# Kernel tuning notes

Hardware: AMD Instinct MI355X
Metric: run time of the kernel (lower is better)

## Reference

```python
import jax, jax.numpy as jnp
import numpy as np

B, L, QD, KVD, H = 8, 1024, 1024, 768, 16
DH = QD // H
EPS = 1e-5


def setup_inputs() -> dict:
    key = jax.random.key(0)
    ks = jax.random.split(key, 12)
    q = jax.random.normal(ks[0], (B, L, QD), jnp.float32)
    k = jax.random.normal(ks[1], (B, L, KVD), jnp.float32)
    v = jax.random.normal(ks[2], (B, L, KVD), jnp.float32)
    # key_padding_mask: True = valid token (code masks where ~mask)
    lengths = jax.random.randint(ks[3], (B,), L // 2, L + 1)
    key_padding_mask = jnp.arange(L)[None, :] < lengths[:, None]
    def lin(kk, fan_in, fan_out):
        bound = 1.0 / np.sqrt(fan_in)
        k1, k2 = jax.random.split(kk)
        W = jax.random.uniform(k1, (fan_out, fan_in), jnp.float32, -bound, bound)
        b = jax.random.uniform(k2, (fan_out,), jnp.float32, -bound, bound)
        return W, b
    Wq, bq = lin(ks[4], QD, QD)
    Wk, bk = lin(ks[5], KVD, QD)
    Wv, bv = lin(ks[6], KVD, QD)
    Wo, bo = lin(ks[7], QD, QD)
    gamma = jnp.ones((QD,), jnp.float32)
    beta = jnp.zeros((QD,), jnp.float32)
    return {"q": q, "k": k, "v": v, "key_padding_mask": key_padding_mask,
            "Wq": Wq, "bq": bq, "Wk": Wk, "bk": bk, "Wv": Wv, "bv": bv,
            "Wo": Wo, "bo": bo, "gamma": gamma, "beta": beta}


def reference(q, k, v, key_padding_mask, Wq, bq, Wk, bk, Wv, bv, Wo, bo, gamma, beta):
    Bq, Lq, C = q.shape
    scale = DH ** -0.5
    # projections -> [B, H, L, DH]
    qh = (q @ Wq.T + bq).reshape(Bq, Lq, H, DH).transpose(0, 2, 1, 3)
    kh = (k @ Wk.T + bk).reshape(Bq, Lq, H, DH).transpose(0, 2, 1, 3)
    vh = (v @ Wv.T + bv).reshape(Bq, Lq, H, DH).transpose(0, 2, 1, 3)
    attn = jnp.einsum('bhld,bhmd->bhlm', qh, kh) * scale
    attn = jnp.where(key_padding_mask[:, None, None, :], attn, -jnp.inf)
    p = jax.nn.softmax(attn, axis=-1)
    out = jnp.einsum('bhlm,bhmd->bhld', p, vh).transpose(0, 2, 1, 3).reshape(Bq, Lq, C)
    out = out @ Wo.T + bo  # dropout is identity in eval
    y = out + q
    mu = jnp.mean(y, axis=-1, keepdims=True)
    var = jnp.var(y, axis=-1, keepdims=True)
    return (y - mu) * jax.lax.rsqrt(var + EPS) * gamma + beta
```

## Files before the change

### kernel.cpp

```cpp
#include <hip/hip_runtime.h>
#include <stdint.h>

typedef float f32x4 __attribute__((ext_vector_type(4)));
typedef __bf16 bf16x8 __attribute__((ext_vector_type(8)));
typedef unsigned short u16;

__device__ __forceinline__ void gload_lds16(const void* g, void* l) {
  __builtin_amdgcn_global_load_lds(
      (__attribute__((address_space(1))) void*)(uintptr_t)(g),
      (__attribute__((address_space(3))) void*)(uint32_t)(uintptr_t)(l),
      16, 0, 0);
}

__device__ __forceinline__ u16 f2bf(float x) {
  __bf16 h = (__bf16)x;
  return *(u16*)&h;
}

__device__ __forceinline__ void barrier_raw() {
  __builtin_amdgcn_sched_barrier(0);
  __builtin_amdgcn_s_barrier();
  __builtin_amdgcn_sched_barrier(0);
}

__global__ __launch_bounds__(256) void cast_all(
    const float* __restrict__ q, const float* __restrict__ k,
    const float* __restrict__ v, const float* __restrict__ wq,
    const float* __restrict__ wk, const float* __restrict__ wv,
    const float* __restrict__ wo, u16* __restrict__ out) {
  const int g = blockIdx.x;
  const float* in;
  int s;
  if (g < 8192) { in = q; s = 0; }
  else if (g < 14336) { in = k; s = 8192; }
  else if (g < 20480) { in = v; s = 14336; }
  else if (g < 21504) { in = wq; s = 20480; }
  else if (g < 22272) { in = wk; s = 21504; }
  else if (g < 23040) { in = wv; s = 22272; }
  else { in = wo; s = 23040; }
  const int li = (g - s) * 256 + threadIdx.x;
  float4 x = *((const float4*)in + li);
  unsigned lo = (unsigned)f2bf(x.x) | ((unsigned)f2bf(x.y) << 16);
  unsigned hi = (unsigned)f2bf(x.z) | ((unsigned)f2bf(x.w) << 16);
  ((uint2*)out)[(size_t)g * 256 + threadIdx.x] = make_uint2(lo, hi);
}

__global__ __launch_bounds__(256) void proj_kernel(
    const u16* __restrict__ qb, const u16* __restrict__ kb,
    const u16* __restrict__ vb, const u16* __restrict__ wqb,
    const u16* __restrict__ wkb, const u16* __restrict__ wvb,
    const float* __restrict__ bq, const float* __restrict__ bk,
    const float* __restrict__ bv, u16* __restrict__ qpb,
    u16* __restrict__ kpb, u16* __restrict__ vtb) {
  __shared__ __align__(16) u16 As[3][128 * 32];
  __shared__ __align__(16) u16 Bs[3][128 * 32];
  const int tid = threadIdx.x;
  const int role = blockIdx.y >> 3;
  const int m0 = blockIdx.x * 128, n0 = (blockIdx.y & 7) * 128;
  const int K = (role == 0) ? 1024 : 768;
  const u16* A = (role == 0) ? qb : ((role == 1) ? kb : vb);
  const u16* Bt = (role == 0) ? wqb : ((role == 1) ? wkb : wvb);
  const float* bias = (role == 0) ? bq : ((role == 1) ? bk : bv);
  const int lane = tid & 63, w = tid >> 6;
  const int wr = w >> 1, wc = w & 1;
  const int l16 = lane & 15, lk = lane >> 4;
  const int srow = tid >> 2, schunk = tid & 3;
  const int nk = K >> 5;

  const u16* Ap = A + (size_t)(m0 + srow) * K + schunk * 8;
  const u16* Bp = Bt + (size_t)(n0 + srow) * K + schunk * 8;

  f32x4 acc[4][4] = {};

#pragma unroll
  for (int t = 0; t < 2; ++t)
#pragma unroll
    for (int p = 0; p < 2; ++p) {
      gload_lds16(Ap + (size_t)p * 64 * K + t * 32, As[t] + tid * 8 + p * 2048);
      gload_lds16(Bp + (size_t)p * 64 * K + t * 32, Bs[t] + tid * 8 + p * 2048);
    }

  int cur = 0;
  for (int kt = 0; kt < nk; ++kt) {
    const int stg = (cur >= 1) ? cur - 1 : 2;
    if (kt + 2 < nk) {
      const int ko = (kt + 2) << 5;
#pragma unroll
      for (int p = 0; p < 2; ++p) {
        gload_lds16(Ap + (size_t)p * 64 * K + ko, As[stg] + tid * 8 + p * 2048);
        gload_lds16(Bp + (size_t)p * 64 * K + ko, Bs[stg] + tid * 8 + p * 2048);
      }
      asm volatile("s_waitcnt vmcnt(8)" ::: "memory");
    } else if (kt + 1 < nk) {
      asm volatile("s_waitcnt vmcnt(4)" ::: "memory");
    } else {
      asm volatile("s_waitcnt vmcnt(0)" ::: "memory");
    }
    barrier_raw();

    bf16x8 a[4], b[4];
#pragma unroll
    for (int i = 0; i < 4; ++i)
      a[i] = *(const bf16x8*)(As[cur] + (wr * 64 + i * 16 + l16) * 32 + lk * 8);
#pragma unroll
    for (int j = 0; j < 4; ++j)
      b[j] = *(const bf16x8*)(Bs[cur] + (wc * 64 + j * 16 + l16) * 32 + lk * 8);
    __builtin_amdgcn_s_setprio(1);
#pragma unroll
    for (int i = 0; i < 4; ++i)
#pragma unroll
      for (int j = 0; j < 4; ++j)
        acc[i][j] = __builtin_amdgcn_mfma_f32_16x16x32_bf16(a[i], b[j], acc[i][j], 0, 0, 0);
    __builtin_amdgcn_s_setprio(0);
    barrier_raw();
    cur = (cur < 2) ? cur + 1 : 0;
  }

#pragma unroll
  for (int i = 0; i < 4; ++i) {
    const int mrow = m0 + wr * 64 + i * 16 + lk * 4;
#pragma unroll
    for (int j = 0; j < 4; ++j) {
      const int col = n0 + wc * 64 + j * 16 + l16;
      const float bval = bias[col];
      if (role == 0) {
#pragma unroll
        for (int r = 0; r < 4; ++r)
          qpb[(size_t)(mrow + r) * 1024 + col] = f2bf(acc[i][j][r] + bval);
      } else if (role == 1) {
#pragma unroll
        for (int r = 0; r < 4; ++r)
          kpb[(size_t)(mrow + r) * 1024 + col] = f2bf(acc[i][j][r] + bval);
      } else {
        const int bb = mrow >> 10, l = mrow & 1023;
        const int hh = col >> 6, dd = col & 63;
        u16 u0 = f2bf(acc[i][j][0] + bval);
        u16 u1 = f2bf(acc[i][j][1] + bval);
        u16 u2 = f2bf(acc[i][j][2] + bval);
        u16 u3 = f2bf(acc[i][j][3] + bval);
        uint2 pkt = make_uint2((unsigned)u0 | ((unsigned)u1 << 16),
                               (unsigned)u2 | ((unsigned)u3 << 16));
        *(uint2*)(vtb + ((size_t)((bb * 16 + hh) * 64 + dd) << 10) + l) = pkt;
      }
    }
  }
}

__global__ __launch_bounds__(256) void attn_kernel(
    const u16* __restrict__ qp, const u16* __restrict__ kp,
    const u16* __restrict__ vt, const int* __restrict__ mask,
    u16* __restrict__ out) {
  __shared__ __align__(16) u16 KV[2][2][64 * 64];
  __shared__ __align__(16) u16 Ps[4][16 * 64];
  const int tid = threadIdx.x;
  const int qt = blockIdx.x, h = blockIdx.y, b = blockIdx.z;
  const int lane = tid & 63, w = tid >> 6;
  const int l16 = lane & 15, lk = lane >> 4;
  const int srow = tid >> 3, schunk = tid & 7;
  const int sw = schunk ^ (srow & 7);

  int cnt = 0;
  {
    const int4* mp = (const int4*)(mask + (b << 10));
#pragma unroll
    for (int i = 0; i < 4; ++i) {
      const int4 mv = mp[lane * 4 + i];
      cnt += (mv.x ? 1 : 0) + (mv.y ? 1 : 0) + (mv.z ? 1 : 0) + (mv.w ? 1 : 0);
    }
#pragma unroll
    for (int off = 1; off < 64; off <<= 1) cnt += __shfl_xor(cnt, off);
  }
  const int ntile = (cnt + 63) >> 6;
  const int rem = cnt & 63;

#pragma unroll
  for (int p = 0; p < 2; ++p) {
    gload_lds16(qp + (((size_t)(b * 1024 + qt * 64 + p * 32 + srow)) << 10) + h * 64 + sw * 8,
                KV[1][0] + tid * 8 + p * 2048);
    gload_lds16(kp + (((size_t)(b * 1024 + p * 32 + srow)) << 10) + h * 64 + sw * 8,
                KV[0][0] + tid * 8 + p * 2048);
    gload_lds16(vt + (((size_t)((b * 16 + h) * 64 + p * 32 + srow)) << 10) + sw * 8,
                KV[0][1] + tid * 8 + p * 2048);
  }
  __syncthreads();
  const int qrow = w * 16 + l16, qs = qrow & 7;
  bf16x8 aq0 = *(const bf16x8*)(KV[1][0] + qrow * 64 + (lk ^ qs) * 8);
  bf16x8 aq1 = *(const bf16x8*)(KV[1][0] + qrow * 64 + ((lk + 4) ^ qs) * 8);
  __syncthreads();

  const float SC2 = 0.18033688011112042f;
  float lsumq = 0.f;
  f32x4 oacc[4] = {};
  const int e7 = l16 & 7;

  int cur = 0;
  for (int kt = 0; kt < ntile; ++kt) {
    if (kt + 1 < ntile) {
#pragma unroll
      for (int p = 0; p < 2; ++p) {
        gload_lds16(kp + (((size_t)(b * 1024 + (kt + 1) * 64 + p * 32 + srow)) << 10) + h * 64 + sw * 8,
                    KV[cur ^ 1][0] + tid * 8 + p * 2048);
        gload_lds16(vt + (((size_t)((b * 16 + h) * 64 + p * 32 + srow)) << 10) + (kt + 1) * 64 + sw * 8,
                    KV[cur ^ 1][1] + tid * 8 + p * 2048);
      }
    }
    const u16* Kb = KV[cur][0];
    const u16* Vb = KV[cur][1];

    f32x4 sfr[4] = {};
    __builtin_amdgcn_s_setprio(1);
#pragma unroll
    for (int nf = 0; nf < 4; ++nf) {
      const int krow = nf * 16 + l16;
      bf16x8 bk0 = *(const bf16x8*)(Kb + krow * 64 + (lk ^ e7) * 8);
      bf16x8 bk1 = *(const bf16x8*)(Kb + krow * 64 + ((lk + 4) ^ e7) * 8);
      sfr[nf] = __builtin_amdgcn_mfma_f32_16x16x32_bf16(bk0, aq0, sfr[nf], 0, 0, 0);
      sfr[nf] = __builtin_amdgcn_mfma_f32_16x16x32_bf16(bk1, aq1, sfr[nf], 0, 0, 0);
    }
    __builtin_amdgcn_s_setprio(0);

    const bool partial = (kt == ntile - 1) && (rem != 0);
    u16* Pw = &Ps[w][0];
#pragma unroll
    for (int nf = 0; nf < 4; ++nf) {
      float pv0 = __builtin_amdgcn_exp2f(sfr[nf][0] * SC2);
      float pv1 = __builtin_amdgcn_exp2f(sfr[nf][1] * SC2);
      float pv2 = __builtin_amdgcn_exp2f(sfr[nf][2] * SC2);
      float pv3 = __builtin_amdgcn_exp2f(sfr[nf][3] * SC2);
      if (partial) {
        const int k0 = nf * 16 + lk * 4;
        pv0 = (k0 + 0 < rem) ? pv0 : 0.f;
        pv1 = (k0 + 1 < rem) ? pv1 : 0.f;
        pv2 = (k0 + 2 < rem) ? pv2 : 0.f;
        pv3 = (k0 + 3 < rem) ? pv3 : 0.f;
      }
      lsumq += (pv0 + pv1) + (pv2 + pv3);
      unsigned lo = (unsigned)f2bf(pv0) | ((unsigned)f2bf(pv1) << 16);
      unsigned hi = (unsigned)f2bf(pv2) | ((unsigned)f2bf(pv3) << 16);
      *(uint2*)(Pw + l16 * 64 + (((nf * 2 + (lk >> 1)) ^ e7) * 8 + (lk & 1) * 4)) =
          make_uint2(lo, hi);
    }

    bf16x8 ap0 = *(const bf16x8*)(Pw + l16 * 64 + ((lk ^ e7) * 8));
    bf16x8 ap1 = *(const bf16x8*)(Pw + l16 * 64 + (((4 + lk) ^ e7) * 8));
    __builtin_amdgcn_s_setprio(1);
#pragma unroll
    for (int nf = 0; nf < 4; ++nf) {
      const int vrow = nf * 16 + l16;
      bf16x8 bv0 = *(const bf16x8*)(Vb + vrow * 64 + (lk ^ e7) * 8);
      bf16x8 bv1 = *(const bf16x8*)(Vb + vrow * 64 + ((lk + 4) ^ e7) * 8);
      oacc[nf] = __builtin_amdgcn_mfma_f32_16x16x32_bf16(ap0, bv0, oacc[nf], 0, 0, 0);
      oacc[nf] = __builtin_amdgcn_mfma_f32_16x16x32_bf16(ap1, bv1, oacc[nf], 0, 0, 0);
    }
    __builtin_amdgcn_s_setprio(0);

    __syncthreads();
    cur ^= 1;
  }

  lsumq += __shfl_xor(lsumq, 16);
  lsumq += __shfl_xor(lsumq, 32);
  float rinv[4];
#pragma unroll
  for (int r = 0; r < 4; ++r) rinv[r] = 1.0f / __shfl(lsumq, lk * 4 + r);

#pragma unroll
  for (int nf = 0; nf < 4; ++nf)
#pragma unroll
    for (int r = 0; r < 4; ++r) {
      const int tok = b * 1024 + qt * 64 + w * 16 + lk * 4 + r;
      const int col = h * 64 + nf * 16 + l16;
      out[((size_t)tok << 10) + col] = f2bf(oacc[nf][r] * rinv[r]);
    }
}

__global__ __launch_bounds__(256) void gemm_o(
    const u16* __restrict__ A, const u16* __restrict__ Bt,
    const float* __restrict__ bias, float* __restrict__ Cf,
    const float* __restrict__ res) {
  __shared__ __align__(16) u16 As[3][128 * 32];
  __shared__ __align__(16) u16 Bs[3][128 * 32];
  const int K = 1024, N = 1024, nk = 32;
  const int tid = threadIdx.x;
  const int m0 = blockIdx.x * 128, n0 = blockIdx.y * 128;
  const int lane = tid & 63, w = tid >> 6;
  const int wr = w >> 1, wc = w & 1;
  const int l16 = lane & 15, lk = lane >> 4;
  const int srow = tid >> 2, schunk = tid & 3;

  const u16* Ap = A + (size_t)(m0 + srow) * K + schunk * 8;
  const u16* Bp = Bt + (size_t)(n0 + srow) * K + schunk * 8;

  f32x4 acc[4][4] = {};

#pragma unroll
  for (int t = 0; t < 2; ++t)
#pragma unroll
    for (int p = 0; p < 2; ++p) {
      gload_lds16(Ap + (size_t)p * 64 * K + t * 32, As[t] + tid * 8 + p * 2048);
      gload_lds16(Bp + (size_t)p * 64 * K + t * 32, Bs[t] + tid * 8 + p * 2048);
    }

  int cur = 0;
  for (int kt = 0; kt < nk; ++kt) {
    const int stg = (cur >= 1) ? cur - 1 : 2;
    if (kt + 2 < nk) {
      const int ko = (kt + 2) << 5;
#pragma unroll
      for (int p = 0; p < 2; ++p) {
        gload_lds16(Ap + (size_t)p * 64 * K + ko, As[stg] + tid * 8 + p * 2048);
        gload_lds16(Bp + (size_t)p * 64 * K + ko, Bs[stg] + tid * 8 + p * 2048);
      }
      asm volatile("s_waitcnt vmcnt(8)" ::: "memory");
    } else if (kt + 1 < nk) {
      asm volatile("s_waitcnt vmcnt(4)" ::: "memory");
    } else {
      asm volatile("s_waitcnt vmcnt(0)" ::: "memory");
    }
    barrier_raw();

    bf16x8 a[4], b[4];
#pragma unroll
    for (int i = 0; i < 4; ++i)
      a[i] = *(const bf16x8*)(As[cur] + (wr * 64 + i * 16 + l16) * 32 + lk * 8);
#pragma unroll
    for (int j = 0; j < 4; ++j)
      b[j] = *(const bf16x8*)(Bs[cur] + (wc * 64 + j * 16 + l16) * 32 + lk * 8);
    __builtin_amdgcn_s_setprio(1);
#pragma unroll
    for (int i = 0; i < 4; ++i)
#pragma unroll
      for (int j = 0; j < 4; ++j)
        acc[i][j] = __builtin_amdgcn_mfma_f32_16x16x32_bf16(a[i], b[j], acc[i][j], 0, 0, 0);
    __builtin_amdgcn_s_setprio(0);
    barrier_raw();
    cur = (cur < 2) ? cur + 1 : 0;
  }

#pragma unroll
  for (int i = 0; i < 4; ++i) {
    const int mrow = m0 + wr * 64 + i * 16 + lk * 4;
#pragma unroll
    for (int j = 0; j < 4; ++j) {
      const int col = n0 + wc * 64 + j * 16 + l16;
      const float bval = bias[col];
#pragma unroll
      for (int r = 0; r < 4; ++r) {
        const size_t idx = (size_t)(mrow + r) * N + col;
        Cf[idx] = acc[i][j][r] + bval + res[idx];
      }
    }
  }
}

__global__ __launch_bounds__(256) void ln_kernel(float* __restrict__ y,
                                                 const float* __restrict__ gamma,
                                                 const float* __restrict__ beta) {
  __shared__ float ssum[4], ssq[4];
  const int tid = threadIdx.x;
  float* yr = y + ((size_t)blockIdx.x << 10);
  float4 v = *((const float4*)yr + tid);
  float s = v.x + v.y + v.z + v.w;
  float q2 = v.x * v.x + v.y * v.y + v.z * v.z + v.w * v.w;
#pragma unroll
  for (int off = 1; off < 64; off <<= 1) {
    s += __shfl_xor(s, off);
    q2 += __shfl_xor(q2, off);
  }
  if ((tid & 63) == 0) { ssum[tid >> 6] = s; ssq[tid >> 6] = q2; }
  __syncthreads();
  s = ssum[0] + ssum[1] + ssum[2] + ssum[3];
  q2 = ssq[0] + ssq[1] + ssq[2] + ssq[3];
  const float mu = s * (1.0f / 1024.0f);
  const float rstd = rsqrtf(q2 * (1.0f / 1024.0f) - mu * mu + 1e-5f);
  float4 g = *((const float4*)gamma + tid);
  float4 be = *((const float4*)beta + tid);
  float4 o;
  o.x = (v.x - mu) * rstd * g.x + be.x;
  o.y = (v.y - mu) * rstd * g.y + be.y;
  o.z = (v.z - mu) * rstd * g.z + be.z;
  o.w = (v.w - mu) * rstd * g.w + be.w;
  *((float4*)yr + tid) = o;
}

extern "C" void kernel_launch(void* const* d_in, const int* in_sizes, int n_in,
                              void* d_out, int out_size, void* d_ws, size_t ws_size,
                              hipStream_t stream) {
  (void)in_sizes; (void)n_in; (void)out_size; (void)ws_size;
  const float* q = (const float*)d_in[0];
  const float* k = (const float*)d_in[1];
  const float* v = (const float*)d_in[2];
  const int* msk = (const int*)d_in[3];
  const float* Wq = (const float*)d_in[4];
  const float* bq = (const float*)d_in[5];
  const float* Wk = (const float*)d_in[6];
  const float* bk = (const float*)d_in[7];
  const float* Wv = (const float*)d_in[8];
  const float* bv = (const float*)d_in[9];
  const float* Wo = (const float*)d_in[10];
  const float* bo = (const float*)d_in[11];
  const float* gamma = (const float*)d_in[12];
  const float* beta = (const float*)d_in[13];
  float* out = (float*)d_out;

  char* p = (char*)d_ws;
  auto take = [&p](size_t bytes) {
    char* r = p;
    p += (bytes + 255) & ~(size_t)255;
    return r;
  };
  u16* qb = (u16*)take(8192ull * 1024 * 2);
  u16* kb = (u16*)take(8192ull * 768 * 2);
  u16* vb = (u16*)take(8192ull * 768 * 2);
  u16* wqb = (u16*)take(1024ull * 1024 * 2);
  u16* wkb = (u16*)take(1024ull * 768 * 2);
  u16* wvb = (u16*)take(1024ull * 768 * 2);
  u16* wob = (u16*)take(1024ull * 1024 * 2);
  u16* qpb = (u16*)take(8192ull * 1024 * 2);
  u16* kpb = (u16*)take(8192ull * 1024 * 2);
  u16* vtb = (u16*)take(8192ull * 1024 * 2);
  u16* atb = (u16*)take(8192ull * 1024 * 2);

  cast_all<<<dim3(24064), 256, 0, stream>>>(q, k, v, Wq, Wk, Wv, Wo, qb);

  proj_kernel<<<dim3(64, 24), 256, 0, stream>>>(qb, kb, vb, wqb, wkb, wvb,
                                                bq, bk, bv, qpb, kpb, vtb);

  attn_kernel<<<dim3(16, 16, 8), 256, 0, stream>>>(qpb, kpb, vtb, msk, atb);

  gemm_o<<<dim3(64, 8), 256, 0, stream>>>(atb, wob, bo, out, q);

  ln_kernel<<<dim3(8192), 256, 0, stream>>>(out, gamma, beta);
}
```

Baseline: 184.8 us.

## Enlarge projection GEMM M-tile to 256 and XOR-swizzle LDS chunks

The QKV projection kernel now computes a 256x128 tile per block, so each warp holds 8x4 accumulators and weight tiles are reused across twice as many rows. The grid shrinks to 32x24 and the wait counts are adjusted for six loads per stage. Both the projection and output GEMMs also XOR-swizzle the 16-byte chunk placement in LDS, applied on the global-to-LDS store and undone on the fragment reads, to reduce LDS bank conflicts. The larger tile raises register and LDS use and halves the number of blocks, which may lower occupancy and load balance.

```diff
diff --git a/kernel.cpp b/kernel.cpp
--- a/kernel.cpp
+++ b/kernel.cpp
@@ -45,18 +45,18 @@
   ((uint2*)out)[(size_t)g * 256 + threadIdx.x] = make_uint2(lo, hi);
 }
 
-__global__ __launch_bounds__(256) void proj_kernel(
+__global__ __launch_bounds__(256, 2) void proj_kernel(
     const u16* __restrict__ qb, const u16* __restrict__ kb,
     const u16* __restrict__ vb, const u16* __restrict__ wqb,
     const u16* __restrict__ wkb, const u16* __restrict__ wvb,
     const float* __restrict__ bq, const float* __restrict__ bk,
     const float* __restrict__ bv, u16* __restrict__ qpb,
     u16* __restrict__ kpb, u16* __restrict__ vtb) {
-  __shared__ __align__(16) u16 As[3][128 * 32];
+  __shared__ __align__(16) u16 As[3][256 * 32];
   __shared__ __align__(16) u16 Bs[3][128 * 32];
   const int tid = threadIdx.x;
   const int role = blockIdx.y >> 3;
-  const int m0 = blockIdx.x * 128, n0 = (blockIdx.y & 7) * 128;
+  const int m0 = blockIdx.x * 256, n0 = (blockIdx.y & 7) * 128;
   const int K = (role == 0) ? 1024 : 768;
   const u16* A = (role == 0) ? qb : ((role == 1) ? kb : vb);
   const u16* Bt = (role == 0) ? wqb : ((role == 1) ? wkb : wvb);
@@ -64,50 +64,51 @@
   const int lane = tid & 63, w = tid >> 6;
   const int wr = w >> 1, wc = w & 1;
   const int l16 = lane & 15, lk = lane >> 4;
-  const int srow = tid >> 2, schunk = tid & 3;
   const int nk = K >> 5;
-
-  const u16* Ap = A + (size_t)(m0 + srow) * K + schunk * 8;
-  const u16* Bp = Bt + (size_t)(n0 + srow) * K + schunk * 8;
-
-  f32x4 acc[4][4] = {};
-
-#pragma unroll
-  for (int t = 0; t < 2; ++t)
-#pragma unroll
-    for (int p = 0; p < 2; ++p) {
-      gload_lds16(Ap + (size_t)p * 64 * K + t * 32, As[t] + tid * 8 + p * 2048);
-      gload_lds16(Bp + (size_t)p * 64 * K + t * 32, Bs[t] + tid * 8 + p * 2048);
-    }
-
+  const int srow = tid >> 2;
+  const int sw = (tid & 3) ^ ((tid >> 3) & 3);
+
+  const u16* Ap = A + (size_t)(m0 + srow) * K + sw * 8;
+  const u16* Bp = Bt + (size_t)(n0 + srow) * K + sw * 8;
+
+  f32x4 acc[8][4] = {};
+
+  auto stage = [&](int t, int ko) {
+#pragma unroll
+    for (int l = 0; l < 4; ++l)
+      gload_lds16(Ap + (size_t)l * 64 * K + ko, As[t] + tid * 8 + l * 2048);
+#pragma unroll
+    for (int l = 0; l < 2; ++l)
+      gload_lds16(Bp + (size_t)l * 64 * K + ko, Bs[t] + tid * 8 + l * 2048);
+  };
+
+  stage(0, 0);
+  stage(1, 32);
+
+  const int e2 = (l16 >> 1) & 3;
   int cur = 0;
   for (int kt = 0; kt < nk; ++kt) {
     const int stg = (cur >= 1) ? cur - 1 : 2;
     if (kt + 2 < nk) {
-      const int ko = (kt + 2) << 5;
-#pragma unroll
-      for (int p = 0; p < 2; ++p) {
-        gload_lds16(Ap + (size_t)p * 64 * K + ko, As[stg] + tid * 8 + p * 2048);
-        gload_lds16(Bp + (size_t)p * 64 * K + ko, Bs[stg] + tid * 8 + p * 2048);
-      }
-      asm volatile("s_waitcnt vmcnt(8)" ::: "memory");
+      stage(stg, (kt + 2) << 5);
+      asm volatile("s_waitcnt vmcnt(12)" ::: "memory");
     } else if (kt + 1 < nk) {
-      asm volatile("s_waitcnt vmcnt(4)" ::: "memory");
+      asm volatile("s_waitcnt vmcnt(6)" ::: "memory");
     } else {
       asm volatile("s_waitcnt vmcnt(0)" ::: "memory");
     }
     barrier_raw();
 
-    bf16x8 a[4], b[4];
-#pragma unroll
-    for (int i = 0; i < 4; ++i)
-      a[i] = *(const bf16x8*)(As[cur] + (wr * 64 + i * 16 + l16) * 32 + lk * 8);
+    bf16x8 a[8], b[4];
+#pragma unroll
+    for (int i = 0; i < 8; ++i)
+      a[i] = *(const bf16x8*)(As[cur] + (wr * 128 + i * 16 + l16) * 32 + (lk ^ e2) * 8);
 #pragma unroll
     for (int j = 0; j < 4; ++j)
-      b[j] = *(const bf16x8*)(Bs[cur] + (wc * 64 + j * 16 + l16) * 32 + lk * 8);
+      b[j] = *(const bf16x8*)(Bs[cur] + (wc * 64 + j * 16 + l16) * 32 + (lk ^ e2) * 8);
     __builtin_amdgcn_s_setprio(1);
 #pragma unroll
-    for (int i = 0; i < 4; ++i)
+    for (int i = 0; i < 8; ++i)
 #pragma unroll
       for (int j = 0; j < 4; ++j)
         acc[i][j] = __builtin_amdgcn_mfma_f32_16x16x32_bf16(a[i], b[j], acc[i][j], 0, 0, 0);
@@ -117,8 +118,8 @@
   }
 
 #pragma unroll
-  for (int i = 0; i < 4; ++i) {
-    const int mrow = m0 + wr * 64 + i * 16 + lk * 4;
+  for (int i = 0; i < 8; ++i) {
+    const int mrow = m0 + wr * 128 + i * 16 + lk * 4;
 #pragma unroll
     for (int j = 0; j < 4; ++j) {
       const int col = n0 + wc * 64 + j * 16 + l16;
@@ -286,10 +287,11 @@
   const int lane = tid & 63, w = tid >> 6;
   const int wr = w >> 1, wc = w & 1;
   const int l16 = lane & 15, lk = lane >> 4;
-  const int srow = tid >> 2, schunk = tid & 3;
-
-  const u16* Ap = A + (size_t)(m0 + srow) * K + schunk * 8;
-  const u16* Bp = Bt + (size_t)(n0 + srow) * K + schunk * 8;
+  const int srow = tid >> 2;
+  const int sw = (tid & 3) ^ ((tid >> 3) & 3);
+
+  const u16* Ap = A + (size_t)(m0 + srow) * K + sw * 8;
+  const u16* Bp = Bt + (size_t)(n0 + srow) * K + sw * 8;
 
   f32x4 acc[4][4] = {};
 
@@ -301,6 +303,7 @@
       gload_lds16(Bp + (size_t)p * 64 * K + t * 32, Bs[t] + tid * 8 + p * 2048);
     }
 
+  const int e2 = (l16 >> 1) & 3;
   int cur = 0;
   for (int kt = 0; kt < nk; ++kt) {
     const int stg = (cur >= 1) ? cur - 1 : 2;
@@ -322,10 +325,10 @@
     bf16x8 a[4], b[4];
 #pragma unroll
     for (int i = 0; i < 4; ++i)
-      a[i] = *(const bf16x8*)(As[cur] + (wr * 64 + i * 16 + l16) * 32 + lk * 8);
+      a[i] = *(const bf16x8*)(As[cur] + (wr * 64 + i * 16 + l16) * 32 + (lk ^ e2) * 8);
 #pragma unroll
     for (int j = 0; j < 4; ++j)
-      b[j] = *(const bf16x8*)(Bs[cur] + (wc * 64 + j * 16 + l16) * 32 + lk * 8);
+      b[j] = *(const bf16x8*)(Bs[cur] + (wc * 64 + j * 16 + l16) * 32 + (lk ^ e2) * 8);
     __builtin_amdgcn_s_setprio(1);
 #pragma unroll
     for (int i = 0; i < 4; ++i)
@@ -423,7 +426,7 @@
 
   cast_all<<<dim3(24064), 256, 0, stream>>>(q, k, v, Wq, Wk, Wv, Wo, qb);
 
-  proj_kernel<<<dim3(64, 24), 256, 0, stream>>>(qb, kb, vb, wqb, wkb, wvb,
+  proj_kernel<<<dim3(32, 24), 256, 0, stream>>>(qb, kb, vb, wqb, wkb, wvb,
                                                 bq, bk, bv, qpb, kpb, vtb);
 
   attn_kernel<<<dim3(16, 16, 8), 256, 0, stream>>>(qpb, kpb, vtb, msk, atb);
```

Result: faster. 179.1 us (-3.1%).
